# Kernel optimization log

Measured on AMD Instinct MI355X. Metric: run time of the kernel, lower is better.

## Reference

```python
import jax, jax.numpy as jnp
import numpy as np
import math

B, Q, K, D = 32, 2048, 2048, 128


def setup_inputs() -> dict:
    key = jax.random.key(0)
    k1, k2, k3, k4 = jax.random.split(key, 4)
    return {
        "queries": jax.random.normal(k1, (B, Q, D), dtype=jnp.float32),
        "keys": jax.random.normal(k2, (B, K, D), dtype=jnp.float32),
        "values": jax.random.normal(k3, (B, K, D), dtype=jnp.float32),
        "valid_len": jax.random.randint(k4, (B,), 0, Q, dtype=jnp.int32),
    }


def reference(queries, keys, values, valid_len):
    d = queries.shape[-1]
    # [B, Q, K] scores
    scores = jnp.einsum("bqd,bkd->bqk", queries, keys) / math.sqrt(d)
    # Faithful to source: mask is over the QUERY dim (X.size(1) of [B,Q,K]);
    # rows with q >= valid_len[b] are set entirely to -1e5 before softmax.
    row_mask = jnp.arange(scores.shape[1]) < valid_len[:, None]  # [B, Q]
    scores = jnp.where(row_mask[:, :, None], scores, -100000.0)
    attn = jax.nn.softmax(scores, axis=-1)  # dropout p=0 -> identity
    return jnp.einsum("bqk,bkv->bqv", attn, values)
```

## Files before the change

### kernel.cpp

```cpp
#include <hip/hip_runtime.h>
#include <stdint.h>

#define NB 32
#define NQ 2048
#define NKK 2048
#define DH 128

constexpr int QBLK = 128;
constexpr int KBLK = 64;
constexpr int NKT  = NKK / KBLK;
constexpr float C2 = 0.12754299817f;

typedef short short8  __attribute__((ext_vector_type(8)));
typedef float f32x4   __attribute__((ext_vector_type(4)));
typedef float f32x16  __attribute__((ext_vector_type(16)));
typedef uint32_t u32x2 __attribute__((ext_vector_type(2)));
typedef uint32_t u32x4 __attribute__((ext_vector_type(4)));

typedef __attribute__((address_space(3))) uint32_t lds_u32_t;
typedef __attribute__((address_space(1))) const uint32_t glb_u32_t;

__device__ __forceinline__ uint16_t f2bf(float x) {
    union { float f; uint32_t u; } v; v.f = x;
    uint32_t r = v.u + 0x7fffu + ((v.u >> 16) & 1u);
    return (uint16_t)(r >> 16);
}

__device__ __forceinline__ void gload16(const void* g, void* l) {
    __builtin_amdgcn_global_load_lds((glb_u32_t*)g, (lds_u32_t*)l, 16, 0, 0);
}

__device__ __forceinline__ uint32_t cvtpk(float lo, float hi) {
    uint32_t d;
    asm("v_cvt_pk_bf16_f32 %0, %1, %2" : "=v"(d) : "v"(lo), "v"(hi));
    return d;
}

__global__ void conv_bf16(const float* __restrict__ in, u32x4* __restrict__ out, int n8) {
    int i = blockIdx.x * blockDim.x + threadIdx.x;
    int stride = gridDim.x * blockDim.x;
    for (; i < n8; i += stride) {
        f32x4 a = ((const f32x4*)in)[2 * i];
        f32x4 b = ((const f32x4*)in)[2 * i + 1];
        u32x4 w;
        w[0] = (uint32_t)f2bf(a[0]) | ((uint32_t)f2bf(a[1]) << 16);
        w[1] = (uint32_t)f2bf(a[2]) | ((uint32_t)f2bf(a[3]) << 16);
        w[2] = (uint32_t)f2bf(b[0]) | ((uint32_t)f2bf(b[1]) << 16);
        w[3] = (uint32_t)f2bf(b[2]) | ((uint32_t)f2bf(b[3]) << 16);
        out[i] = w;
    }
}

__global__ void transpose_v(const float* __restrict__ V, uint16_t* __restrict__ Vt) {
    __shared__ uint16_t T[64][72];
    const int bid = blockIdx.x;
    const int dt = bid & 1;
    const int kt = (bid >> 1) & 31;
    const int b  = bid >> 6;
    const int tid = threadIdx.x;
    const float* src = V + ((size_t)(b * NKK + kt * 64)) * DH + dt * 64;
    #pragma unroll
    for (int i = 0; i < 4; ++i) {
        int flat = i * 256 + tid;
        int kr = flat >> 4;
        int c4 = (flat & 15) * 4;
        f32x4 x = *(const f32x4*)(src + (size_t)kr * DH + c4);
        T[c4 + 0][kr] = f2bf(x[0]);
        T[c4 + 1][kr] = f2bf(x[1]);
        T[c4 + 2][kr] = f2bf(x[2]);
        T[c4 + 3][kr] = f2bf(x[3]);
    }
    __syncthreads();
    uint16_t* dst = Vt + ((size_t)b * DH + dt * 64) * NKK + kt * 64;
    #pragma unroll
    for (int i = 0; i < 4; ++i) {
        int flat = i * 256 + tid;
        int dr = flat >> 4;
        int c4 = (flat & 15) * 4;
        u32x2 w;
        w[0] = (uint32_t)T[dr][c4 + 0] | ((uint32_t)T[dr][c4 + 1] << 16);
        w[1] = (uint32_t)T[dr][c4 + 2] | ((uint32_t)T[dr][c4 + 3] << 16);
        *(u32x2*)(dst + (size_t)dr * NKK + c4) = w;
    }
}

__global__ __launch_bounds__(256, 2)
void attn_fwd(const float* __restrict__ Qg, const uint16_t* __restrict__ Kb,
              const uint16_t* __restrict__ Vtb, const int* __restrict__ VL,
              float* __restrict__ Og) {
    __shared__ __align__(16) uint16_t KT[2][KBLK * DH];
    __shared__ __align__(16) uint16_t VT[2][DH * KBLK];

    const int tid  = threadIdx.x;
    const int wv   = tid >> 6;
    const int lane = tid & 63;
    const int m    = lane & 31;
    const int h    = lane >> 5;

    const int bid = blockIdx.x;
    const int swz = (bid & 7) * 64 + (bid >> 3);
    const int b   = swz >> 4;
    const int qt  = swz & 15;
    const int qb0 = qt * QBLK + wv * 32;

    const int vlen = VL[b];
    const float sc = ((qb0 + m) < vlen) ? C2 : 0.0f;

    short8 qf[8];
    {
        const float* qp = Qg + ((size_t)b * NQ + qb0 + m) * DH;
        #pragma unroll
        for (int t = 0; t < 8; ++t) {
            const float* p = qp + t * 16 + h * 8;
            f32x4 x0 = *(const f32x4*)(p);
            f32x4 x1 = *(const f32x4*)(p + 4);
            short8 f;
            f[0] = f2bf(x0[0]); f[1] = f2bf(x0[1]); f[2] = f2bf(x0[2]); f[3] = f2bf(x0[3]);
            f[4] = f2bf(x1[0]); f[5] = f2bf(x1[1]); f[6] = f2bf(x1[2]); f[7] = f2bf(x1[3]);
            qf[t] = f;
        }
    }

    f32x16 oacc[4];
    #pragma unroll
    for (int n = 0; n < 4; ++n)
        #pragma unroll
        for (int r = 0; r < 16; ++r) oacc[n][r] = 0.0f;
    float lsum = 0.0f;

    const char* kbase = (const char*)(Kb + (size_t)b * NKK * DH);
    const char* vbase = (const char*)(Vtb + (size_t)b * DH * NKK);

    auto stage = [&](int buf, int ktile) {
        const char* ks = kbase + (size_t)ktile * KBLK * DH * 2;
        #pragma unroll
        for (int i = 0; i < 4; ++i) {
            int ob = (i * 4 + wv) * 1024 + lane * 16;
            int row = ob >> 8;
            gload16(ks + (ob ^ ((row & 7) << 4)), (char*)&KT[buf][0] + ob);
        }
        const char* vs = vbase + (size_t)ktile * KBLK * 2;
        #pragma unroll
        for (int i = 0; i < 4; ++i) {
            int ob = (i * 4 + wv) * 1024 + lane * 16;
            int row = ob >> 7;
            int cb = ob & 127;
            gload16(vs + (size_t)row * (NKK * 2) + (cb ^ ((row & 7) << 4)),
                    (char*)&VT[buf][0] + ob);
        }
    };

    stage(0, 0);
    __syncthreads();

    int cur = 0;
    for (int kt = 0; kt < NKT; ++kt) {
        if (kt + 1 < NKT) stage(cur ^ 1, kt + 1);

        f32x16 sacc[2];
        #pragma unroll
        for (int ct = 0; ct < 2; ++ct)
            #pragma unroll
            for (int r = 0; r < 16; ++r) sacc[ct][r] = 0.0f;
        #pragma unroll
        for (int ct = 0; ct < 2; ++ct) {
            const int row = ct * 32 + m;
            const int sw = (row & 7) << 4;
            #pragma unroll
            for (int t = 0; t < 8; ++t) {
                int ob = row * 256 + ((t * 32 + h * 16) ^ sw);
                short8 kf = *(const short8*)((const char*)&KT[cur][0] + ob);
                sacc[ct] = __builtin_amdgcn_mfma_f32_32x32x16_bf16(kf, qf[t], sacc[ct], 0, 0, 0);
            }
        }

        short8 pa[4];
        #pragma unroll
        for (int u = 0; u < 4; ++u) {
            const int ci = u >> 1;
            const int r0 = (u & 1) * 8;
            float p[8];
            #pragma unroll
            for (int j = 0; j < 8; ++j)
                p[j] = __builtin_amdgcn_exp2f(sacc[ci][r0 + j] * sc);
            lsum += ((p[0] + p[1]) + (p[2] + p[3])) + ((p[4] + p[5]) + (p[6] + p[7]));
            union { uint32_t w[4]; short8 s; } pu;
            pu.w[0] = cvtpk(p[0], p[1]);
            pu.w[1] = cvtpk(p[2], p[3]);
            pu.w[2] = cvtpk(p[4], p[5]);
            pu.w[3] = cvtpk(p[6], p[7]);
            pa[u] = pu.s;
        }

        #pragma unroll
        for (int nt = 0; nt < 4; ++nt) {
            const int row = nt * 32 + m;
            const int sw = (row & 7) << 4;
            const char* vrow = (const char*)&VT[cur][0] + row * 128;
            #pragma unroll
            for (int u = 0; u < 4; ++u) {
                const int ci = u >> 1;
                const int uu = u & 1;
                int c0 = (ci * 64 + uu * 32 + h * 8) ^ sw;
                union { u32x2 u2[2]; short8 s; } vv;
                vv.u2[0] = *(const u32x2*)(vrow + c0);
                vv.u2[1] = *(const u32x2*)(vrow + (c0 ^ 16));
                oacc[nt] = __builtin_amdgcn_mfma_f32_32x32x16_bf16(pa[u], vv.s, oacc[nt], 0, 0, 0);
            }
        }

        __syncthreads();
        cur ^= 1;
    }

    float ltot = lsum + __shfl_xor(lsum, 32);
    float* op = Og + ((size_t)b * NQ + qb0) * DH;
    #pragma unroll
    for (int r = 0; r < 16; ++r) {
        const int qr = (r & 3) + 8 * (r >> 2) + 4 * h;
        float lv = __shfl(ltot, qr);
        float inv = 1.0f / lv;
        #pragma unroll
        for (int nt = 0; nt < 4; ++nt)
            op[(size_t)qr * DH + nt * 32 + m] = oacc[nt][r] * inv;
    }
}

extern "C" void kernel_launch(void* const* d_in, const int* in_sizes, int n_in,
                              void* d_out, int out_size, void* d_ws, size_t ws_size,
                              hipStream_t stream) {
    const float* q  = (const float*)d_in[0];
    const float* k  = (const float*)d_in[1];
    const float* v  = (const float*)d_in[2];
    const int*   vl = (const int*)d_in[3];
    float* out = (float*)d_out;

    uint16_t* Kb  = (uint16_t*)d_ws;
    uint16_t* Vtb = Kb + (size_t)NB * NKK * DH;

    conv_bf16<<<2048, 256, 0, stream>>>(k, (u32x4*)Kb, NB * NKK * DH / 8);
    transpose_v<<<2048, 256, 0, stream>>>(v, Vtb);
    attn_fwd<<<NB * (NQ / QBLK), 256, 0, stream>>>(q, Kb, Vtb, vl, out);
}
```

Baseline: 106.5 us.

## Pre-pack K and V into MFMA fragment order for conflict-free LDS reads

The preprocessing kernels now write K and V in bf16, already arranged in the per-lane MFMA fragment order for each 64-key tile. The attention kernel can then stage tiles with straight contiguous 16-byte global-to-LDS copies and read each fragment with one 16-byte LDS load per lane, with no XOR swizzle arithmetic and no split 8-byte V reads. The aim is fewer LDS instructions and less address math in the inner loop. The trade-off is that conv_vf does strided scalar fp32 reads of V with no shared-memory transpose, which could make the preprocessing step slower.

```diff
diff --git a/kernel.cpp b/kernel.cpp
--- a/kernel.cpp
+++ b/kernel.cpp
@@ -14,7 +14,6 @@
 typedef short short8  __attribute__((ext_vector_type(8)));
 typedef float f32x4   __attribute__((ext_vector_type(4)));
 typedef float f32x16  __attribute__((ext_vector_type(16)));
-typedef uint32_t u32x2 __attribute__((ext_vector_type(2)));
 typedef uint32_t u32x4 __attribute__((ext_vector_type(4)));
 
 typedef __attribute__((address_space(3))) uint32_t lds_u32_t;
@@ -36,60 +35,65 @@
     return d;
 }
 
-__global__ void conv_bf16(const float* __restrict__ in, u32x4* __restrict__ out, int n8) {
-    int i = blockIdx.x * blockDim.x + threadIdx.x;
-    int stride = gridDim.x * blockDim.x;
-    for (; i < n8; i += stride) {
-        f32x4 a = ((const f32x4*)in)[2 * i];
-        f32x4 b = ((const f32x4*)in)[2 * i + 1];
-        u32x4 w;
-        w[0] = (uint32_t)f2bf(a[0]) | ((uint32_t)f2bf(a[1]) << 16);
-        w[1] = (uint32_t)f2bf(a[2]) | ((uint32_t)f2bf(a[3]) << 16);
-        w[2] = (uint32_t)f2bf(b[0]) | ((uint32_t)f2bf(b[1]) << 16);
-        w[3] = (uint32_t)f2bf(b[2]) | ((uint32_t)f2bf(b[3]) << 16);
-        out[i] = w;
-    }
-}
-
-__global__ void transpose_v(const float* __restrict__ V, uint16_t* __restrict__ Vt) {
-    __shared__ uint16_t T[64][72];
+__global__ void conv_kf(const float* __restrict__ K, uint16_t* __restrict__ Kf) {
+    __shared__ __align__(16) uint16_t T[64][136];
     const int bid = blockIdx.x;
-    const int dt = bid & 1;
-    const int kt = (bid >> 1) & 31;
-    const int b  = bid >> 6;
+    const int b = bid >> 5, kt = bid & 31;
     const int tid = threadIdx.x;
-    const float* src = V + ((size_t)(b * NKK + kt * 64)) * DH + dt * 64;
-    #pragma unroll
-    for (int i = 0; i < 4; ++i) {
-        int flat = i * 256 + tid;
-        int kr = flat >> 4;
-        int c4 = (flat & 15) * 4;
-        f32x4 x = *(const f32x4*)(src + (size_t)kr * DH + c4);
-        T[c4 + 0][kr] = f2bf(x[0]);
-        T[c4 + 1][kr] = f2bf(x[1]);
-        T[c4 + 2][kr] = f2bf(x[2]);
-        T[c4 + 3][kr] = f2bf(x[3]);
+    const float* src = K + ((size_t)(b * NKK + kt * 64)) * DH;
+    #pragma unroll
+    for (int r = 0; r < 8; ++r) {
+        int flat = r * 256 + tid;
+        int row = flat >> 5;
+        int c4 = (flat & 31) * 4;
+        f32x4 x = *(const f32x4*)(src + (size_t)row * DH + c4);
+        T[row][c4 + 0] = f2bf(x[0]);
+        T[row][c4 + 1] = f2bf(x[1]);
+        T[row][c4 + 2] = f2bf(x[2]);
+        T[row][c4 + 3] = f2bf(x[3]);
     }
     __syncthreads();
-    uint16_t* dst = Vt + ((size_t)b * DH + dt * 64) * NKK + kt * 64;
-    #pragma unroll
-    for (int i = 0; i < 4; ++i) {
-        int flat = i * 256 + tid;
-        int dr = flat >> 4;
-        int c4 = (flat & 15) * 4;
-        u32x2 w;
-        w[0] = (uint32_t)T[dr][c4 + 0] | ((uint32_t)T[dr][c4 + 1] << 16);
-        w[1] = (uint32_t)T[dr][c4 + 2] | ((uint32_t)T[dr][c4 + 3] << 16);
-        *(u32x2*)(dst + (size_t)dr * NKK + c4) = w;
+    uint16_t* dst = Kf + (size_t)bid * 8192;
+    #pragma unroll
+    for (int r = 0; r < 4; ++r) {
+        int c = r * 256 + tid;
+        int s = c >> 6, lane = c & 63;
+        int ci = s >> 3, t = s & 7;
+        int mm = lane & 31, hh = lane >> 5;
+        short8 v = *(const short8*)&T[ci * 32 + mm][t * 16 + hh * 8];
+        *(short8*)(dst + (size_t)c * 8) = v;
+    }
+}
+
+__global__ void conv_vf(const float* __restrict__ V, uint16_t* __restrict__ Vf) {
+    const int bid = blockIdx.x;
+    const int b = bid >> 5, kt = bid & 31;
+    const int tid = threadIdx.x;
+    const float* src = V + (size_t)b * NKK * DH;
+    uint16_t* dst = Vf + (size_t)bid * 8192;
+    #pragma unroll
+    for (int r = 0; r < 4; ++r) {
+        int c = r * 256 + tid;
+        int s = c >> 6, lane = c & 63;
+        int ci = s >> 3, nt = (s >> 1) & 3, uu = s & 1;
+        int m = lane & 31, h = lane >> 5;
+        int kb = kt * 64 + ci * 32 + uu * 16 + 4 * h;
+        int d = nt * 32 + m;
+        short8 w;
+        #pragma unroll
+        for (int j = 0; j < 8; ++j) {
+            int key = kb + (j & 3) + 8 * (j >> 2);
+            w[j] = (short)f2bf(src[(size_t)key * DH + d]);
+        }
+        *(short8*)(dst + (size_t)c * 8) = w;
     }
 }
 
 __global__ __launch_bounds__(256, 2)
-void attn_fwd(const float* __restrict__ Qg, const uint16_t* __restrict__ Kb,
-              const uint16_t* __restrict__ Vtb, const int* __restrict__ VL,
+void attn_fwd(const float* __restrict__ Qg, const uint16_t* __restrict__ Kf,
+              const uint16_t* __restrict__ Vf, const int* __restrict__ VL,
               float* __restrict__ Og) {
-    __shared__ __align__(16) uint16_t KT[2][KBLK * DH];
-    __shared__ __align__(16) uint16_t VT[2][DH * KBLK];
+    __shared__ __align__(16) uint8_t LB[65536];
 
     const int tid  = threadIdx.x;
     const int wv   = tid >> 6;
@@ -123,30 +127,23 @@
 
     f32x16 oacc[4];
     #pragma unroll
-    for (int n = 0; n < 4; ++n)
-        #pragma unroll
-        for (int r = 0; r < 16; ++r) oacc[n][r] = 0.0f;
+    for (int nt = 0; nt < 4; ++nt)
+        #pragma unroll
+        for (int r = 0; r < 16; ++r) oacc[nt][r] = 0.0f;
     float lsum = 0.0f;
 
-    const char* kbase = (const char*)(Kb + (size_t)b * NKK * DH);
-    const char* vbase = (const char*)(Vtb + (size_t)b * DH * NKK);
+    const char* kfb = (const char*)Kf + (size_t)b * 32 * 16384;
+    const char* vfb = (const char*)Vf + (size_t)b * 32 * 16384;
 
     auto stage = [&](int buf, int ktile) {
-        const char* ks = kbase + (size_t)ktile * KBLK * DH * 2;
-        #pragma unroll
-        for (int i = 0; i < 4; ++i) {
-            int ob = (i * 4 + wv) * 1024 + lane * 16;
-            int row = ob >> 8;
-            gload16(ks + (ob ^ ((row & 7) << 4)), (char*)&KT[buf][0] + ob);
-        }
-        const char* vs = vbase + (size_t)ktile * KBLK * 2;
-        #pragma unroll
-        for (int i = 0; i < 4; ++i) {
-            int ob = (i * 4 + wv) * 1024 + lane * 16;
-            int row = ob >> 7;
-            int cb = ob & 127;
-            gload16(vs + (size_t)row * (NKK * 2) + (cb ^ ((row & 7) << 4)),
-                    (char*)&VT[buf][0] + ob);
+        const char* ks = kfb + (size_t)ktile * 16384;
+        const char* vs = vfb + (size_t)ktile * 16384;
+        char* kd = (char*)LB + buf * 16384;
+        char* vd = (char*)LB + 32768 + buf * 16384;
+        #pragma unroll
+        for (int r = 0; r < 4; ++r) {
+            gload16(ks + r * 4096 + tid * 16, kd + r * 4096 + tid * 16);
+            gload16(vs + r * 4096 + tid * 16, vd + r * 4096 + tid * 16);
         }
     };
 
@@ -156,21 +153,20 @@
     int cur = 0;
     for (int kt = 0; kt < NKT; ++kt) {
         if (kt + 1 < NKT) stage(cur ^ 1, kt + 1);
+        const char* KTc = (const char*)LB + cur * 16384 + (size_t)lane * 16;
+        const char* VTc = (const char*)LB + 32768 + cur * 16384 + (size_t)lane * 16;
 
         f32x16 sacc[2];
         #pragma unroll
-        for (int ct = 0; ct < 2; ++ct)
-            #pragma unroll
-            for (int r = 0; r < 16; ++r) sacc[ct][r] = 0.0f;
-        #pragma unroll
-        for (int ct = 0; ct < 2; ++ct) {
-            const int row = ct * 32 + m;
-            const int sw = (row & 7) << 4;
+        for (int ci = 0; ci < 2; ++ci)
+            #pragma unroll
+            for (int r = 0; r < 16; ++r) sacc[ci][r] = 0.0f;
+        #pragma unroll
+        for (int ci = 0; ci < 2; ++ci) {
             #pragma unroll
             for (int t = 0; t < 8; ++t) {
-                int ob = row * 256 + ((t * 32 + h * 16) ^ sw);
-                short8 kf = *(const short8*)((const char*)&KT[cur][0] + ob);
-                sacc[ct] = __builtin_amdgcn_mfma_f32_32x32x16_bf16(kf, qf[t], sacc[ct], 0, 0, 0);
+                short8 kf = *(const short8*)(KTc + (ci * 8 + t) * 1024);
+                sacc[ci] = __builtin_amdgcn_mfma_f32_32x32x16_bf16(kf, qf[t], sacc[ci], 0, 0, 0);
             }
         }
 
@@ -194,18 +190,12 @@
 
         #pragma unroll
         for (int nt = 0; nt < 4; ++nt) {
-            const int row = nt * 32 + m;
-            const int sw = (row & 7) << 4;
-            const char* vrow = (const char*)&VT[cur][0] + row * 128;
             #pragma unroll
             for (int u = 0; u < 4; ++u) {
                 const int ci = u >> 1;
                 const int uu = u & 1;
-                int c0 = (ci * 64 + uu * 32 + h * 8) ^ sw;
-                union { u32x2 u2[2]; short8 s; } vv;
-                vv.u2[0] = *(const u32x2*)(vrow + c0);
-                vv.u2[1] = *(const u32x2*)(vrow + (c0 ^ 16));
-                oacc[nt] = __builtin_amdgcn_mfma_f32_32x32x16_bf16(pa[u], vv.s, oacc[nt], 0, 0, 0);
+                short8 vfr = *(const short8*)(VTc + (ci * 8 + nt * 2 + uu) * 1024);
+                oacc[nt] = __builtin_amdgcn_mfma_f32_32x32x16_bf16(pa[u], vfr, oacc[nt], 0, 0, 0);
             }
         }
 
@@ -235,10 +225,10 @@
     const int*   vl = (const int*)d_in[3];
     float* out = (float*)d_out;
 
-    uint16_t* Kb  = (uint16_t*)d_ws;
-    uint16_t* Vtb = Kb + (size_t)NB * NKK * DH;
-
-    conv_bf16<<<2048, 256, 0, stream>>>(k, (u32x4*)Kb, NB * NKK * DH / 8);
-    transpose_v<<<2048, 256, 0, stream>>>(v, Vtb);
-    attn_fwd<<<NB * (NQ / QBLK), 256, 0, stream>>>(q, Kb, Vtb, vl, out);
-}
+    uint16_t* Kf = (uint16_t*)d_ws;
+    uint16_t* Vf = Kf + (size_t)NB * NKT * 8192;
+
+    conv_kf<<<NB * NKT, 256, 0, stream>>>(k, Kf);
+    conv_vf<<<NB * NKT, 256, 0, stream>>>(v, Vf);
+    attn_fwd<<<NB * (NQ / QBLK), 256, 0, stream>>>(q, Kf, Vf, vl, out);
+}
```

Result: faster. 90.51 us (-15.0%).
